# Optimization experiments

Hardware: AMD Instinct MI355X
Metric: run time of the kernel (lower is better)

## Reference

```python
import jax, jax.numpy as jnp
import numpy as np

# Model dims (scaled Mistral-style decoder)
L = 2        # layers
D = 2048     # d_model
H = 16       # query heads
HK = 4       # kv heads (GQA)
HD = 128     # head dim
F = 8192     # SwiGLU hidden
V = 32000    # vocab
R = 64       # LoRA rank
BATCH = 16
S = 128
BLK = 64             # NF4 quant blocksize
SCALE = 128.0 / 64.0  # lora_alpha / r
THETA = 10000.0
EPS = 1e-5

# bitsandbytes NF4 codebook (16 levels)
NF4 = jnp.array([-1.0, -0.6961928009986877, -0.5250730514526367, -0.39491748809814453,
                 -0.28444138169288635, -0.18477343022823334, -0.09105003625154495, 0.0,
                 0.07958029955625534, 0.16093020141124725, 0.24611230194568634,
                 0.33791524171829224, 0.44070982933044434, 0.5626170039176941,
                 0.7229568362236023, 1.0], dtype=jnp.float32)


def _dequant(codes, absmax):
    # codes: [out, in] int codes 0..15; absmax: [out, in//BLK] per-block scale
    o, i = codes.shape
    w = NF4[codes].reshape(o, i // BLK, BLK) * absmax[:, :, None]
    return w.reshape(o, i)


def _qlinear(x, codes, absmax, A, Bm):
    # fused NF4 dequant + GEMM + LoRA delta: y = x W^T + scale * (x A^T) B^T
    return x @ _dequant(codes, absmax).T + SCALE * ((x @ A.T) @ Bm.T)


def _rms(x, w):
    return x * jax.lax.rsqrt(jnp.mean(x * x, axis=-1, keepdims=True) + EPS) * w


def _rope(x):
    # x: [B, S, heads, HD]; rotate-half RoPE
    half = HD // 2
    inv = 1.0 / (THETA ** (jnp.arange(half, dtype=jnp.float32) / half))
    ang = jnp.arange(x.shape[1], dtype=jnp.float32)[:, None] * inv[None, :]  # [S, half]
    cos = jnp.cos(ang)[None, :, None, :]
    sin = jnp.sin(ang)[None, :, None, :]
    x1, x2 = x[..., :half], x[..., half:]
    return jnp.concatenate([x1 * cos - x2 * sin, x2 * cos + x1 * sin], axis=-1)


def reference(input_ids, attention_mask, embed, attn_norm_w, mlp_norm_w, final_norm_w,
              q_codes, q_absmax, q_A, q_B, k_codes, k_absmax, k_A, k_B,
              v_codes, v_absmax, v_A, v_B, o_codes, o_absmax, o_A, o_B,
              gate_codes, gate_absmax, gate_A, gate_B, up_codes, up_absmax, up_A, up_B,
              down_codes, down_absmax, down_A, down_B):
    b, s = input_ids.shape
    h = embed[input_ids]  # [B, S, D]
    causal = jnp.tril(jnp.ones((s, s), dtype=bool))
    keep = causal[None, None, :, :] & (attention_mask[:, None, None, :] > 0)
    bias = jnp.where(keep, 0.0, -1e9).astype(h.dtype)
    for l in range(L):
        x = _rms(h, attn_norm_w[l])
        q = _qlinear(x, q_codes[l], q_absmax[l], q_A[l], q_B[l]).reshape(b, s, H, HD)
        k = _qlinear(x, k_codes[l], k_absmax[l], k_A[l], k_B[l]).reshape(b, s, HK, HD)
        v = _qlinear(x, v_codes[l], v_absmax[l], v_A[l], v_B[l]).reshape(b, s, HK, HD)
        q = _rope(q)
        k = _rope(k)
        k = jnp.repeat(k, H // HK, axis=2)  # GQA expand
        v = jnp.repeat(v, H // HK, axis=2)
        scores = jnp.einsum('bqhd,bkhd->bhqk', q, k) / jnp.sqrt(jnp.float32(HD)) + bias
        attn = jax.nn.softmax(scores, axis=-1)
        ctx = jnp.einsum('bhqk,bkhd->bqhd', attn, v).reshape(b, s, D)
        h = h + _qlinear(ctx, o_codes[l], o_absmax[l], o_A[l], o_B[l])
        x = _rms(h, mlp_norm_w[l])
        g = _qlinear(x, gate_codes[l], gate_absmax[l], gate_A[l], gate_B[l])
        u = _qlinear(x, up_codes[l], up_absmax[l], up_A[l], up_B[l])
        h = h + _qlinear(jax.nn.silu(g) * u, down_codes[l], down_absmax[l], down_A[l], down_B[l])
    h = _rms(h, final_norm_w)
    # last-token pooling: gather hidden state at sum(mask)-1 (normalized=False)
    seq_len = jnp.sum(attention_mask, axis=1) - 1
    return h[jnp.arange(b), seq_len]


def setup_inputs() -> dict:
    key = jax.random.key(0)
    ks = iter(jax.random.split(key, 64))
    def codes(shape):
        return jax.random.randint(next(ks), shape, 0, 16, dtype=jnp.int32)
    def absm(o, i):
        return jax.random.uniform(next(ks), (L, o, i // BLK), dtype=jnp.float32) * 0.05
    def lora(o, i):
        A = jax.random.normal(next(ks), (L, R, i), dtype=jnp.float32) * 0.02
        Bm = jax.random.normal(next(ks), (L, o, R), dtype=jnp.float32) * 0.02
        return A, Bm
    inp = {
        'input_ids': jax.random.randint(next(ks), (BATCH, S), 0, V, dtype=jnp.int32),
        'attention_mask': jnp.ones((BATCH, S), dtype=jnp.int32),
        'embed': jax.random.normal(next(ks), (V, D), dtype=jnp.float32) * 0.02,
        'attn_norm_w': jnp.ones((L, D), jnp.float32),
        'mlp_norm_w': jnp.ones((L, D), jnp.float32),
        'final_norm_w': jnp.ones((D,), jnp.float32),
    }
    dims = {'q': (D, D), 'k': (HK * HD, D), 'v': (HK * HD, D), 'o': (D, D),
            'gate': (F, D), 'up': (F, D), 'down': (D, F)}
    for name, (o, i) in dims.items():
        A, Bm = lora(o, i)
        inp[f'{name}_codes'] = codes((L, o, i))
        inp[f'{name}_absmax'] = absm(o, i)
        inp[f'{name}_A'] = A
        inp[f'{name}_B'] = Bm
    return inp
```

## Files before the change

### kernel.cpp

```cpp
#include <hip/hip_runtime.h>
#include <stdint.h>

#define D_ 2048
#define H_ 16
#define HK_ 4
#define F_ 8192
#define R_ 64
#define NTOK_ 2048
#define EPS_ 1e-5f

typedef unsigned short u16;
typedef short short8 __attribute__((ext_vector_type(8)));
typedef float f32x4 __attribute__((ext_vector_type(4)));

__constant__ float NF4_TAB[16] = {
  -1.0f, -0.6961928009986877f, -0.5250730514526367f, -0.39491748809814453f,
  -0.28444138169288635f, -0.18477343022823334f, -0.09105003625154495f, 0.0f,
  0.07958029955625534f, 0.16093020141124725f, 0.24611230194568634f, 0.33791524171829224f,
  0.44070982933044434f, 0.5626170039176941f, 0.7229568362236023f, 1.0f };

static __device__ __forceinline__ float b2f(u16 u){ return __uint_as_float(((unsigned)u)<<16); }
static __device__ __forceinline__ u16 f2b(float f){
  unsigned u = __float_as_uint(f);
  return (u16)((u + 0x7fffu + ((u>>16)&1u)) >> 16);
}

__global__ void k_embed(const int* __restrict__ ids, const float* __restrict__ embed,
                        float* __restrict__ h){
  int tok = blockIdx.x;
  int id  = ids[tok];
  const float4* src = (const float4*)(embed + (size_t)id * D_);
  float4* dst = (float4*)(h + (size_t)tok * D_);
  for (int i = threadIdx.x; i < D_/4; i += 256) dst[i] = src[i];
}

__global__ void k_rms(const float* __restrict__ h, const float* __restrict__ w,
                      u16* __restrict__ xb){
  __shared__ float red[4];
  int row = blockIdx.x, t = threadIdx.x;
  const float* hr = h + (size_t)row * D_;
  float ss = 0.f;
  for (int i = t; i < D_; i += 256){ float v = hr[i]; ss += v*v; }
  #pragma unroll
  for (int m = 32; m; m >>= 1) ss += __shfl_xor(ss, m, 64);
  if ((t & 63) == 0) red[t >> 6] = ss;
  __syncthreads();
  float sc = rsqrtf((red[0]+red[1]+red[2]+red[3]) * (1.0f/D_) + EPS_);
  for (int i = t; i < D_; i += 256) xb[(size_t)row*D_ + i] = f2b(hr[i]*sc*w[i]);
}

struct FoldSet { const int* c; const float* am; const float* A; const float* Bm; u16* W; };

static __device__ __forceinline__ void fold_tile(const int* __restrict__ codes,
    const float* __restrict__ absmax, const float* __restrict__ Amat,
    const float* __restrict__ Bmat, u16* __restrict__ W, int I, int n0, int k0){
  __shared__ float Cl[64*132];
  __shared__ float nf4s[16];
  u16* At = (u16*)Cl;
  u16* Bl = (u16*)Cl + 128*64;
  int t = threadIdx.x;
  if (t < 16) nf4s[t] = NF4_TAB[t];
  #pragma unroll
  for (int it = 0; it < 8; ++it){
    int fi = it*256 + t;
    int r = fi >> 5, c4 = fi & 31;
    float4 v = *(const float4*)(Amat + (size_t)r*I + k0 + c4*4);
    int kc0 = c4*4;
    At[((kc0+0)*64 + r) ^ (((kc0+0)&7)<<3)] = f2b(v.x);
    At[((kc0+1)*64 + r) ^ (((kc0+1)&7)<<3)] = f2b(v.y);
    At[((kc0+2)*64 + r) ^ (((kc0+2)&7)<<3)] = f2b(v.z);
    At[((kc0+3)*64 + r) ^ (((kc0+3)&7)<<3)] = f2b(v.w);
  }
  #pragma unroll
  for (int it = 0; it < 8; ++it){
    int fi = it*256 + t;
    int nl = fi >> 4, r4 = fi & 15;
    float4 v = *(const float4*)(Bmat + (size_t)(n0+nl)*R_ + r4*4);
    uint2 p; p.x = (unsigned)f2b(v.x) | ((unsigned)f2b(v.y)<<16);
    p.y = (unsigned)f2b(v.z) | ((unsigned)f2b(v.w)<<16);
    *(uint2*)&Bl[(nl*64 + r4*4) ^ ((nl&7)<<3)] = p;
  }
  __syncthreads();
  int w = t >> 6, lane = t & 63;
  int lr = lane & 15, lg = lane >> 4;
  f32x4 acc[2][8];
  #pragma unroll
  for (int mt = 0; mt < 2; ++mt)
    #pragma unroll
    for (int nt = 0; nt < 8; ++nt) acc[mt][nt] = (f32x4){0.f,0.f,0.f,0.f};
  #pragma unroll
  for (int ks = 0; ks < 64; ks += 32){
    short8 af[2], bf_[8];
    #pragma unroll
    for (int mt = 0; mt < 2; ++mt)
      af[mt] = *(const short8*)&At[((w*32 + mt*16 + lr)*64 + ks + lg*8) ^ ((lr&7)<<3)];
    #pragma unroll
    for (int nt = 0; nt < 8; ++nt)
      bf_[nt] = *(const short8*)&Bl[((nt*16 + lr)*64 + ks + lg*8) ^ ((lr&7)<<3)];
    #pragma unroll
    for (int mt = 0; mt < 2; ++mt)
      #pragma unroll
      for (int nt = 0; nt < 8; ++nt)
        acc[mt][nt] = __builtin_amdgcn_mfma_f32_16x16x32_bf16(af[mt], bf_[nt], acc[mt][nt], 0, 0, 0);
  }
  int tk = t & 15, tn2 = t >> 4;
  int Ib = I >> 6;
  int kcb = k0 + tk*8;
  int kblk = kcb >> 6;
  #pragma unroll
  for (int half = 0; half < 2; ++half){
    __syncthreads();
    #pragma unroll
    for (int mt = 0; mt < 2; ++mt)
      #pragma unroll
      for (int nt2 = 0; nt2 < 4; ++nt2)
        *(f32x4*)&Cl[(nt2*16 + lr)*132 + w*32 + mt*16 + lg*4] = acc[mt][half*4 + nt2];
    __syncthreads();
    #pragma unroll
    for (int j = 0; j < 4; ++j){
      int nl = tn2*4 + j;
      int n = n0 + half*64 + nl;
      float am = absmax[(size_t)n*Ib + kblk];
      int4 c0 = *(const int4*)(codes + (size_t)n*I + kcb);
      int4 c1 = *(const int4*)(codes + (size_t)n*I + kcb + 4);
      const float* L = &Cl[nl*132 + tk*8];
      u16 o[8];
      o[0]=f2b(nf4s[c0.x&15]*am + 2.0f*L[0]);
      o[1]=f2b(nf4s[c0.y&15]*am + 2.0f*L[1]);
      o[2]=f2b(nf4s[c0.z&15]*am + 2.0f*L[2]);
      o[3]=f2b(nf4s[c0.w&15]*am + 2.0f*L[3]);
      o[4]=f2b(nf4s[c1.x&15]*am + 2.0f*L[4]);
      o[5]=f2b(nf4s[c1.y&15]*am + 2.0f*L[5]);
      o[6]=f2b(nf4s[c1.z&15]*am + 2.0f*L[6]);
      o[7]=f2b(nf4s[c1.w&15]*am + 2.0f*L[7]);
      uint4 pk;
      pk.x=(unsigned)o[0]|((unsigned)o[1]<<16); pk.y=(unsigned)o[2]|((unsigned)o[3]<<16);
      pk.z=(unsigned)o[4]|((unsigned)o[5]<<16); pk.w=(unsigned)o[6]|((unsigned)o[7]<<16);
      *(uint4*)(W + (size_t)n*I + kcb) = pk;
    }
  }
}

__global__ __launch_bounds__(256) void k_fold3(FoldSet a, FoldSet b, FoldSet c,
                                               int y1, int y2, int I){
  int y = blockIdx.y;
  FoldSet s = (y < y1) ? a : (y < y2) ? b : c;
  int n0 = (y < y1) ? y*128 : (y < y2) ? (y-y1)*128 : (y-y2)*128;
  fold_tile(s.c, s.am, s.A, s.Bm, s.W, I, n0, blockIdx.x*128);
}

#define LDW_ 40
template<int EPI>
__global__ __launch_bounds__(256,3) void k_gemm(const u16* __restrict__ A,
      const u16* __restrict__ B, float* __restrict__ Cf, u16* __restrict__ C0,
      u16* __restrict__ C1, u16* __restrict__ C2, int M, int N, int K){
  __shared__ u16 SA[2][128*LDW_];
  __shared__ u16 SB[2][128*LDW_];
  int t = threadIdx.x;
  int n0 = blockIdx.x*128, m0 = blockIdx.y*128;
  int w = t >> 6, lane = t & 63;
  int mw = (w >> 1)*64, nw = (w & 1)*64;
  int lr = lane & 15, lg = lane >> 4;
  f32x4 acc[4][4];
  #pragma unroll
  for (int mt = 0; mt < 4; ++mt)
    #pragma unroll
    for (int nt = 0; nt < 4; ++nt) acc[mt][nt] = (f32x4){0.f,0.f,0.f,0.f};
  const u16* Ag = A + (size_t)(m0 + (t>>2))*K + (t&3)*8;
  const u16* Bg = B + (size_t)(n0 + (t>>2))*K + (t&3)*8;
  int trow = t >> 2, tcol = (t & 3)*8;
  int wof0 = trow*LDW_ + tcol;
  int wof1 = (64 + trow)*LDW_ + tcol;
  int niter = K >> 5;

  uint4 ra0, ra1, rb0, rb1;
  uint4 sa0, sa1, sb0, sb1;
  auto gload = [&](int it, uint4& a0, uint4& a1, uint4& b0, uint4& b1){
    int kb = it*32;
    a0 = *(const uint4*)(Ag + kb);
    a1 = *(const uint4*)(Ag + (size_t)64*K + kb);
    b0 = *(const uint4*)(Bg + kb);
    b1 = *(const uint4*)(Bg + (size_t)64*K + kb);
  };
  gload(0, ra0, ra1, rb0, rb1);
  gload(1, sa0, sa1, sb0, sb1);

  auto step = [&](int buf, uint4& a0, uint4& a1, uint4& b0, uint4& b1, int pf){
    *(uint4*)&SA[buf][wof0] = a0;
    *(uint4*)&SA[buf][wof1] = a1;
    *(uint4*)&SB[buf][wof0] = b0;
    *(uint4*)&SB[buf][wof1] = b1;
    __builtin_amdgcn_s_waitcnt(0xC07F);
    __builtin_amdgcn_s_barrier();
    gload(pf, a0, a1, b0, b1);
    short8 af[4], bf_[4];
    #pragma unroll
    for (int mt = 0; mt < 4; ++mt) af[mt]  = *(const short8*)&SA[buf][(mw + mt*16 + lr)*LDW_ + lg*8];
    #pragma unroll
    for (int nt = 0; nt < 4; ++nt) bf_[nt] = *(const short8*)&SB[buf][(nw + nt*16 + lr)*LDW_ + lg*8];
    #pragma unroll
    for (int mt = 0; mt < 4; ++mt)
      #pragma unroll
      for (int nt = 0; nt < 4; ++nt)
        acc[mt][nt] = __builtin_amdgcn_mfma_f32_16x16x32_bf16(af[mt], bf_[nt], acc[mt][nt], 0, 0, 0);
  };

  for (int k = 0; k < niter; k += 2){
    step(0, ra0, ra1, rb0, rb1, (k+2 < niter) ? k+2 : k);
    step(1, sa0, sa1, sb0, sb1, (k+3 < niter) ? k+3 : k+1);
  }

  u16* cb_ = C0; int ldc = N; int coff = n0;
  if (EPI == 2){
    if (n0 < 2048)      { cb_ = C0; ldc = 2048; coff = n0; }
    else if (n0 < 2560) { cb_ = C1; ldc = 512;  coff = n0 - 2048; }
    else                { cb_ = C2; ldc = 512;  coff = n0 - 2560; }
  }
  if (EPI == 3){
    if (n0 < 512)       { cb_ = C1; ldc = 512;  coff = n0; }
    else                { cb_ = C2; ldc = 512;  coff = n0 - 512; }
  }
  #pragma unroll
  for (int mt = 0; mt < 4; ++mt)
    #pragma unroll
    for (int nt = 0; nt < 4; ++nt){
      int cl = nw + nt*16 + lr;
      #pragma unroll
      for (int rg = 0; rg < 4; ++rg){
        int row = m0 + mw + mt*16 + lg*4 + rg;
        float v = acc[mt][nt][rg];
        if (EPI == 1){
          Cf[(size_t)row*N + n0 + cl] += v;
        } else if (EPI == 4){
          size_t idx = (size_t)row*ldc + coff + cl;
          float g = b2f(C1[idx]);
          cb_[idx] = f2b((g/(1.0f+__expf(-g)))*v);
        } else {
          cb_[(size_t)row*ldc + coff + cl] = f2b(v);
        }
      }
    }
}

template<int OUT, int GA, int KC>
__global__ __launch_bounds__(256) void k_skinny(const u16* __restrict__ A,
      const u16* __restrict__ B, float* __restrict__ Hf, u16* __restrict__ Cb,
      const int* __restrict__ rows, int N, int K){
  int w = threadIdx.x >> 6, lane = threadIdx.x & 63;
  int lr = lane & 15, lg = lane >> 4;
  int n0 = blockIdx.x*64 + w*16;
  int kbase = blockIdx.y * KC;
  int ar = GA ? rows[lr] : lr;
  f32x4 ac0 = (f32x4){0.f,0.f,0.f,0.f};
  f32x4 ac1 = (f32x4){0.f,0.f,0.f,0.f};
  const u16* Ap = A + (size_t)ar*K + kbase + lg*8;
  const u16* Bp = B + (size_t)(n0 + lr)*K + kbase + lg*8;
  #pragma unroll 8
  for (int k = 0; k < KC; k += 64){
    ac0 = __builtin_amdgcn_mfma_f32_16x16x32_bf16(*(const short8*)(Ap + k),
            *(const short8*)(Bp + k), ac0, 0, 0, 0);
    ac1 = __builtin_amdgcn_mfma_f32_16x16x32_bf16(*(const short8*)(Ap + k + 32),
            *(const short8*)(Bp + k + 32), ac1, 0, 0, 0);
  }
  f32x4 acc = ac0 + ac1;
  #pragma unroll
  for (int rg = 0; rg < 4; ++rg){
    int m = lg*4 + rg;
    if (OUT == 0){
      Cb[(size_t)m*N + n0 + lr] = f2b(acc[rg]);
    } else if (OUT == 1){
      atomicAdd(&Hf[(size_t)rows[m]*D_ + n0 + lr], acc[rg]);
    } else {
      size_t idx = (size_t)m*N + n0 + lr;
      float g = b2f(Cb[idx]);
      Cb[idx] = f2b((g/(1.0f+__expf(-g)))*acc[rg]);
    }
  }
}

__global__ void k_rows(const int* __restrict__ mask, int* __restrict__ rows){
  int b = threadIdx.x;
  if (b < 16){
    int c = 0;
    for (int i = 0; i < 128; ++i) c += (mask[b*128+i] > 0);
    rows[b] = b*128 + c - 1;
  }
}

__global__ void k_rms16(const float* __restrict__ h, const float* __restrict__ w,
                        const int* __restrict__ rows, u16* __restrict__ xq){
  __shared__ float red[4];
  int m = blockIdx.x, t = threadIdx.x;
  const float* hr = h + (size_t)rows[m] * D_;
  float ss = 0.f;
  for (int i = t; i < D_; i += 256){ float v = hr[i]; ss += v*v; }
  #pragma unroll
  for (int mm = 32; mm; mm >>= 1) ss += __shfl_xor(ss, mm, 64);
  if ((t & 63) == 0) red[t >> 6] = ss;
  __syncthreads();
  float sc = rsqrtf((red[0]+red[1]+red[2]+red[3]) * (1.0f/D_) + EPS_);
  for (int i = t; i < D_; i += 256) xq[(size_t)m*D_ + i] = f2b(hr[i]*sc*w[i]);
}

__global__ void k_rope(u16* __restrict__ x, int nh){
  int i = blockIdx.x*256 + threadIdx.x;
  int d = i & 63; int rem = i >> 6; int hh = rem % nh; int tok = rem / nh;
  int s = tok & 127;
  size_t base = (size_t)tok*nh*128 + hh*128 + d;
  float x1 = b2f(x[base]), x2 = b2f(x[base+64]);
  float inv = exp2f(-(float)d * 0.20762050581352868f);
  float ang = (float)s * inv;
  float sn = sinf(ang), cs = cosf(ang);
  x[base]      = f2b(x1*cs - x2*sn);
  x[base+64]   = f2b(x2*cs + x1*sn);
}

__global__ void k_rope16(u16* __restrict__ x, const int* __restrict__ rows){
  int i = blockIdx.x*256 + threadIdx.x;
  int d = i & 63; int hh = (i >> 6) & 15; int m = i >> 10;
  int s = rows[m] & 127;
  size_t base = (size_t)m*2048 + hh*128 + d;
  float x1 = b2f(x[base]), x2 = b2f(x[base+64]);
  float inv = exp2f(-(float)d * 0.20762050581352868f);
  float ang = (float)s * inv;
  float sn = sinf(ang), cs = cosf(ang);
  x[base]      = f2b(x1*cs - x2*sn);
  x[base+64]   = f2b(x2*cs + x1*sn);
}

#define ALD_ 132
__global__ __launch_bounds__(256) void k_attn(const u16* __restrict__ q,
      const u16* __restrict__ kk, const u16* __restrict__ vv,
      const int* __restrict__ mask, u16* __restrict__ ctx){
  __shared__ u16 QP[128*ALD_];
  __shared__ u16 KV[128*ALD_];
  int b = blockIdx.y, h = blockIdx.x;
  int t = threadIdx.x, w = t >> 6, lane = t & 63;
  int lr = lane & 15, lg = lane >> 4;
  #pragma unroll
  for (int it = 0; it < 8; ++it){
    int fi = it*256 + t; int s = fi >> 4, c8 = fi & 15;
    *(uint4*)&QP[s*ALD_ + c8*8] = *(const uint4*)(q  + (size_t)(b*128+s)*2048 + h*128 + c8*8);
    *(uint4*)&KV[s*ALD_ + c8*8] = *(const uint4*)(kk + (size_t)(b*128+s)*512 + (h>>2)*128 + c8*8);
  }
  __syncthreads();
  f32x4 sac[2][8];
  #pragma unroll
  for (int mt = 0; mt < 2; ++mt)
    #pragma unroll
    for (int nt = 0; nt < 8; ++nt) sac[mt][nt] = (f32x4){0.f,0.f,0.f,0.f};
  for (int ks = 0; ks < 128; ks += 32){
    short8 a[2], bb[8];
    #pragma unroll
    for (int mt = 0; mt < 2; ++mt) a[mt] = *(const short8*)&QP[(w*32 + mt*16 + lr)*ALD_ + ks + lg*8];
    #pragma unroll
    for (int nt = 0; nt < 8; ++nt) bb[nt] = *(const short8*)&KV[(nt*16 + lr)*ALD_ + ks + lg*8];
    #pragma unroll
    for (int mt = 0; mt < 2; ++mt)
      #pragma unroll
      for (int nt = 0; nt < 8; ++nt)
        sac[mt][nt] = __builtin_amdgcn_mfma_f32_16x16x32_bf16(a[mt], bb[nt], sac[mt][nt], 0, 0, 0);
  }
  const float NEG = -1e9f, scl = 0.08838834764831845f;
  float mbias[8];
  #pragma unroll
  for (int nt = 0; nt < 8; ++nt) mbias[nt] = (mask[b*128 + nt*16 + lr] > 0) ? 0.f : NEG;
  #pragma unroll
  for (int mt = 0; mt < 2; ++mt)
    #pragma unroll
    for (int rg = 0; rg < 4; ++rg){
      int row = w*32 + mt*16 + lg*4 + rg;
      float vvv[8]; float mx = -3e38f;
      #pragma unroll
      for (int nt = 0; nt < 8; ++nt){
        int col = nt*16 + lr;
        float s_ = sac[mt][nt][rg]*scl + ((col <= row) ? mbias[nt] : NEG);
        vvv[nt] = s_; mx = fmaxf(mx, s_);
      }
      #pragma unroll
      for (int m_ = 1; m_ < 16; m_ <<= 1) mx = fmaxf(mx, __shfl_xor(mx, m_, 64));
      float sum = 0.f;
      #pragma unroll
      for (int nt = 0; nt < 8; ++nt){ vvv[nt] = __expf(vvv[nt]-mx); sum += vvv[nt]; }
      #pragma unroll
      for (int m_ = 1; m_ < 16; m_ <<= 1) sum += __shfl_xor(sum, m_, 64);
      float inv = 1.0f/sum;
      #pragma unroll
      for (int nt = 0; nt < 8; ++nt) QP[row*ALD_ + nt*16 + lr] = f2b(vvv[nt]*inv);
    }
  __syncthreads();
  #pragma unroll
  for (int it = 0; it < 8; ++it){
    int fi = it*256 + t; int s = fi >> 4, c8 = fi & 15;
    u16 tmp[8];
    *(uint4*)tmp = *(const uint4*)(vv + (size_t)(b*128+s)*512 + (h>>2)*128 + c8*8);
    #pragma unroll
    for (int j = 0; j < 8; ++j) KV[(c8*8+j)*ALD_ + s] = tmp[j];
  }
  __syncthreads();
  f32x4 oac[2][8];
  #pragma unroll
  for (int mt = 0; mt < 2; ++mt)
    #pragma unroll
    for (int nt = 0; nt < 8; ++nt) oac[mt][nt] = (f32x4){0.f,0.f,0.f,0.f};
  for (int ks = 0; ks < 128; ks += 32){
    short8 a[2], bb[8];
    #pragma unroll
    for (int mt = 0; mt < 2; ++mt) a[mt] = *(const short8*)&QP[(w*32 + mt*16 + lr)*ALD_ + ks + lg*8];
    #pragma unroll
    for (int nt = 0; nt < 8; ++nt) bb[nt] = *(const short8*)&KV[(nt*16 + lr)*ALD_ + ks + lg*8];
    #pragma unroll
    for (int mt = 0; mt < 2; ++mt)
      #pragma unroll
      for (int nt = 0; nt < 8; ++nt)
        oac[mt][nt] = __builtin_amdgcn_mfma_f32_16x16x32_bf16(a[mt], bb[nt], oac[mt][nt], 0, 0, 0);
  }
  #pragma unroll
  for (int mt = 0; mt < 2; ++mt)
    #pragma unroll
    for (int nt = 0; nt < 8; ++nt)
      #pragma unroll
      for (int rg = 0; rg < 4; ++rg){
        int row = w*32 + mt*16 + lg*4 + rg;
        int col = nt*16 + lr;
        ctx[(size_t)(b*128+row)*2048 + h*128 + col] = f2b(oac[mt][nt][rg]);
      }
}

__global__ void k_attn1(const u16* __restrict__ qc, const u16* __restrict__ kk,
      const u16* __restrict__ vv, const int* __restrict__ mask,
      const int* __restrict__ rows, u16* __restrict__ out){
  __shared__ float ps[128];
  __shared__ float red2[2];
  int h = blockIdx.x, b = blockIdx.y, t = threadIdx.x;
  int pos = rows[b] & 127;
  const u16* qrow = qc + (size_t)b*2048 + h*128;
  const u16* krow = kk + (size_t)(b*128 + t)*512 + (h>>2)*128;
  float acc = 0.f;
  #pragma unroll
  for (int d0 = 0; d0 < 128; d0 += 8){
    short8 qa = *(const short8*)(qrow + d0);
    short8 ka = *(const short8*)(krow + d0);
    #pragma unroll
    for (int j = 0; j < 8; ++j) acc += b2f((u16)qa[j]) * b2f((u16)ka[j]);
  }
  bool keep = (t <= pos) && (mask[b*128 + t] > 0);
  float s_ = keep ? acc * 0.08838834764831845f : -1e9f;
  float mx = s_;
  #pragma unroll
  for (int m_ = 1; m_ < 64; m_ <<= 1) mx = fmaxf(mx, __shfl_xor(mx, m_, 64));
  if ((t & 63) == 0) red2[t >> 6] = mx;
  __syncthreads();
  mx = fmaxf(red2[0], red2[1]);
  float p = __expf(s_ - mx);
  float sum = p;
  #pragma unroll
  for (int m_ = 1; m_ < 64; m_ <<= 1) sum += __shfl_xor(sum, m_, 64);
  __syncthreads();
  if ((t & 63) == 0) red2[t >> 6] = sum;
  __syncthreads();
  float inv = 1.f / (red2[0] + red2[1]);
  ps[t] = p * inv;
  __syncthreads();
  float o = 0.f;
  const u16* vbase = vv + (size_t)b*128*512 + (h>>2)*128 + t;
  for (int s = 0; s < 128; s += 4){
    o += ps[s]   * b2f(vbase[(size_t)(s  )*512]);
    o += ps[s+1] * b2f(vbase[(size_t)(s+1)*512]);
    o += ps[s+2] * b2f(vbase[(size_t)(s+2)*512]);
    o += ps[s+3] * b2f(vbase[(size_t)(s+3)*512]);
  }
  out[(size_t)b*2048 + h*128 + t] = f2b(o);
}

__global__ void k_final(const float* __restrict__ h, const int* __restrict__ mask,
                        const float* __restrict__ w, float* __restrict__ out){
  __shared__ float red[4]; __shared__ int rowsh;
  int b = blockIdx.x, t = threadIdx.x;
  if (t == 0){
    int c = 0;
    for (int i = 0; i < 128; ++i) c += (mask[b*128+i] > 0);
    rowsh = b*128 + c - 1;
  }
  __syncthreads();
  const float* hr = h + (size_t)rowsh*D_;
  float ss = 0.f;
  for (int i = t; i < D_; i += 256){ float x = hr[i]; ss += x*x; }
  #pragma unroll
  for (int m = 32; m; m >>= 1) ss += __shfl_xor(ss, m, 64);
  if ((t & 63) == 0) red[t >> 6] = ss;
  __syncthreads();
  float sc = rsqrtf((red[0]+red[1]+red[2]+red[3]) * (1.0f/D_) + EPS_);
  for (int i = t; i < D_; i += 256) out[(size_t)b*D_ + i] = hr[i]*sc*w[i];
}

extern "C" void kernel_launch(void* const* d_in, const int* in_sizes, int n_in,
                              void* d_out, int out_size, void* d_ws, size_t ws_size,
                              hipStream_t stream) {
  const int*   ids       = (const int*)  d_in[0];
  const int*   mask      = (const int*)  d_in[1];
  const float* embed     = (const float*)d_in[2];
  const float* attn_norm = (const float*)d_in[3];
  const float* mlp_norm  = (const float*)d_in[4];
  const float* fin_norm  = (const float*)d_in[5];
  struct QW { const int* c; const float* am; const float* A; const float* B; };
  auto qw = [&](int i){ return QW{(const int*)d_in[i], (const float*)d_in[i+1],
                                  (const float*)d_in[i+2], (const float*)d_in[i+3]}; };
  QW Wq = qw(6), Wk = qw(10), Wv = qw(14), Wo = qw(18), Wg = qw(22), Wu = qw(26), Wd = qw(30);

  char* ws = (char*)d_ws;
  float* h  = (float*)(ws);
  u16* xb   = (u16*)(ws + 16777216);
  u16* qb   = (u16*)(ws + 25165824);
  u16* kb_  = (u16*)(ws + 33554432);
  u16* vb   = (u16*)(ws + 35651584);
  u16* gb   = (u16*)(ws + 37748736);
  u16* Wb   = (u16*)(ws + 104857600);
  int* rowsi = (int*)(ws + 138412032);
  u16* xq    = (u16*)(ws + 138413056);
  u16* qc    = (u16*)(ws + 138478592);
  u16* cc    = (u16*)(ws + 138544128);
  u16* g16   = (u16*)(ws + 138609664);
  u16* Wb2   = (u16*)(ws + 167772160);

  auto fs = [&](QW W_, int l, int O, int I, u16* dst){
    return FoldSet{ W_.c + (size_t)l*O*I, W_.am + (size_t)l*O*(I>>6),
                    W_.A + (size_t)l*R_*I, W_.B + (size_t)l*O*R_, dst };
  };

  k_embed<<<NTOK_, 256, 0, stream>>>(ids, embed, h);

  for (int l = 0; l < 2; ++l){
    k_rms<<<NTOK_, 256, 0, stream>>>(h, attn_norm + l*D_, xb);
    {
      FoldSet fq = fs(Wq, l, D_, D_, Wb);
      FoldSet fk = fs(Wk, l, 512, D_, Wb + (size_t)2048*D_);
      FoldSet fv = fs(Wv, l, 512, D_, Wb + (size_t)2560*D_);
      k_fold3<<<dim3(16,24), 256, 0, stream>>>(fq, fk, fv, 16, 20, D_);
    }

    if (l == 0){
      k_gemm<2><<<dim3(24,16), 256, 0, stream>>>(xb, Wb, nullptr, qb, kb_, vb, NTOK_, 3072, D_);
      k_rope<<<8192, 256, 0, stream>>>(qb, H_);
      k_rope<<<2048, 256, 0, stream>>>(kb_, HK_);
      k_attn<<<dim3(16,16), 256, 0, stream>>>(qb, kb_, vb, mask, xb);
      {
        FoldSet fo = fs(Wo, l, D_, D_, Wb);
        k_fold3<<<dim3(16,16), 256, 0, stream>>>(fo, fo, fo, 9999, 9999, D_);
      }
      k_gemm<1><<<dim3(16,16), 256, 0, stream>>>(xb, Wb, h, nullptr, nullptr, nullptr, NTOK_, D_, D_);
      k_rms<<<NTOK_, 256, 0, stream>>>(h, mlp_norm + l*D_, xb);
      {
        FoldSet fg = fs(Wg, l, F_, D_, Wb);
        FoldSet fu = fs(Wu, l, F_, D_, Wb2);
        k_fold3<<<dim3(16,128), 256, 0, stream>>>(fg, fu, fu, 64, 64, D_);
      }
      k_gemm<0><<<dim3(64,16), 256, 0, stream>>>(xb, Wb,  nullptr, gb, nullptr, nullptr, NTOK_, F_, D_);
      k_gemm<4><<<dim3(64,16), 256, 0, stream>>>(xb, Wb2, nullptr, gb, gb, nullptr, NTOK_, F_, D_);
      {
        FoldSet fd = fs(Wd, l, D_, F_, Wb);
        k_fold3<<<dim3(64,16), 256, 0, stream>>>(fd, fd, fd, 9999, 9999, F_);
      }
      k_gemm<1><<<dim3(16,16), 256, 0, stream>>>(gb, Wb, h, nullptr, nullptr, nullptr, NTOK_, D_, F_);
    } else {
      k_gemm<3><<<dim3(8,16), 256, 0, stream>>>(xb, Wb + (size_t)2048*D_, nullptr, nullptr,
          kb_, vb, NTOK_, 1024, D_);
      k_rows<<<1, 64, 0, stream>>>(mask, rowsi);
      k_skinny<0,1,2048><<<dim3(32,1), 256, 0, stream>>>(xb, Wb, nullptr, qc, rowsi, D_, D_);
      k_rope16<<<64, 256, 0, stream>>>(qc, rowsi);
      k_rope<<<2048, 256, 0, stream>>>(kb_, HK_);
      k_attn1<<<dim3(16,16), 128, 0, stream>>>(qc, kb_, vb, mask, rowsi, cc);
      {
        FoldSet fo = fs(Wo, l, D_, D_, Wb);
        k_fold3<<<dim3(16,16), 256, 0, stream>>>(fo, fo, fo, 9999, 9999, D_);
      }
      k_skinny<1,0,2048><<<dim3(32,1), 256, 0, stream>>>(cc, Wb, h, nullptr, rowsi, D_, D_);
      k_rms16<<<16, 256, 0, stream>>>(h, mlp_norm + l*D_, rowsi, xq);
      {
        FoldSet fg = fs(Wg, l, F_, D_, Wb);
        FoldSet fu = fs(Wu, l, F_, D_, Wb2);
        k_fold3<<<dim3(16,128), 256, 0, stream>>>(fg, fu, fu, 64, 64, D_);
      }
      k_skinny<0,0,2048><<<dim3(128,1), 256, 0, stream>>>(xq, Wb,  nullptr, g16, rowsi, F_, D_);
      k_skinny<3,0,2048><<<dim3(128,1), 256, 0, stream>>>(xq, Wb2, nullptr, g16, rowsi, F_, D_);
      {
        FoldSet fd = fs(Wd, l, D_, F_, Wb);
        k_fold3<<<dim3(64,16), 256, 0, stream>>>(fd, fd, fd, 9999, 9999, F_);
      }
      k_skinny<1,0,2048><<<dim3(32,4), 256, 0, stream>>>(g16, Wb, h, nullptr, rowsi, D_, F_);
    }
  }
  k_final<<<16, 256, 0, stream>>>(h, mask, fin_norm, (float*)d_out);
}
```

Before: 1.303 ms.

## Add 256x256-tile double-buffered GEMM for layer-0 gate/up projections

Adds a new bf16 MFMA GEMM kernel that uses 256x256 output tiles with 512 threads and a double-buffered, XOR-swizzled LDS layout. Global loads for the next k-step are prefetched into registers while the current step computes, and MFMA issue is wrapped in s_setprio. The layer-0 gate and up GEMMs, including the SiLU-multiply epilogue, now use this kernel, and the EPI==4 path is removed from the old GEMM. The aim is more reuse per LDS load and better latency hiding on the largest GEMMs, at the cost of one block per CU under high register and LDS pressure.

```diff
diff --git a/kernel.cpp b/kernel.cpp
--- a/kernel.cpp
+++ b/kernel.cpp
@@ -231,12 +231,112 @@
         float v = acc[mt][nt][rg];
         if (EPI == 1){
           Cf[(size_t)row*N + n0 + cl] += v;
-        } else if (EPI == 4){
-          size_t idx = (size_t)row*ldc + coff + cl;
-          float g = b2f(C1[idx]);
-          cb_[idx] = f2b((g/(1.0f+__expf(-g)))*v);
         } else {
           cb_[(size_t)row*ldc + coff + cl] = f2b(v);
+        }
+      }
+    }
+}
+
+template<int EPI>
+__global__ __launch_bounds__(512,1) void k_gemm256(const u16* __restrict__ A,
+      const u16* __restrict__ B, u16* __restrict__ C0, const u16* __restrict__ C1,
+      int M, int N, int K){
+  __shared__ u16 LB[2][2][256*64];
+  int t = threadIdx.x;
+  int w = t >> 6, l = t & 63;
+  int wm = w >> 2, wn = w & 3;
+  int lr = l & 15, lg = l >> 4;
+  int ls = l >> 3;
+  int lc = (l & 7)*8;
+  int n0 = blockIdx.x*256, m0 = blockIdx.y*256;
+  f32x4 acc[8][4];
+  #pragma unroll
+  for (int i = 0; i < 8; ++i)
+    #pragma unroll
+    for (int j = 0; j < 4; ++j) acc[i][j] = (f32x4){0.f,0.f,0.f,0.f};
+
+  const u16* Ag = A + (size_t)(m0 + w*8 + ls)*K + lc;
+  const u16* Bg = B + (size_t)(n0 + w*8 + ls)*K + lc;
+  int wrow = w*8 + ls;
+  int wcol = lc ^ ((ls & 7) << 3);
+  int nk = K >> 6;
+
+  uint4 rA[4], rB[4];
+  auto gload = [&](int kt){
+    #pragma unroll
+    for (int i = 0; i < 4; ++i){
+      rA[i] = *(const uint4*)(Ag + (size_t)i*64*K + kt*64);
+      rB[i] = *(const uint4*)(Bg + (size_t)i*64*K + kt*64);
+    }
+  };
+  gload(0);
+
+  for (int kt = 0; kt < nk; ++kt){
+    int buf = kt & 1;
+    u16* As = &LB[buf][0][0];
+    u16* Bs = &LB[buf][1][0];
+    #pragma unroll
+    for (int i = 0; i < 4; ++i){
+      *(uint4*)&As[(i*64 + wrow)*64 + wcol] = rA[i];
+      *(uint4*)&Bs[(i*64 + wrow)*64 + wcol] = rB[i];
+    }
+    __builtin_amdgcn_s_waitcnt(0xC07F);
+    __builtin_amdgcn_s_barrier();
+    gload(kt+1 < nk ? kt+1 : kt);
+
+    short8 aF[4][2], bF[2][2];
+    auto loadA = [&](int pm){
+      #pragma unroll
+      for (int mf = 0; mf < 4; ++mf){
+        int row = wm*128 + pm*64 + mf*16 + lr;
+        #pragma unroll
+        for (int ks = 0; ks < 2; ++ks)
+          aF[mf][ks] = *(const short8*)&As[row*64 + ((ks*32 + lg*8) ^ ((row&7)<<3))];
+      }
+    };
+    auto loadB = [&](int pn){
+      #pragma unroll
+      for (int nf = 0; nf < 2; ++nf){
+        int row = wn*64 + pn*32 + nf*16 + lr;
+        #pragma unroll
+        for (int ks = 0; ks < 2; ++ks)
+          bF[nf][ks] = *(const short8*)&Bs[row*64 + ((ks*32 + lg*8) ^ ((row&7)<<3))];
+      }
+    };
+    auto mma = [&](int pm, int pn){
+      __builtin_amdgcn_s_setprio(1);
+      #pragma unroll
+      for (int mf = 0; mf < 4; ++mf)
+        #pragma unroll
+        for (int nf = 0; nf < 2; ++nf)
+          #pragma unroll
+          for (int ks = 0; ks < 2; ++ks)
+            acc[pm*4+mf][pn*2+nf] = __builtin_amdgcn_mfma_f32_16x16x32_bf16(
+                aF[mf][ks], bF[nf][ks], acc[pm*4+mf][pn*2+nf], 0, 0, 0);
+      __builtin_amdgcn_s_setprio(0);
+    };
+    loadA(0); loadB(0); mma(0, 0);
+    loadA(1);           mma(1, 0);
+    loadB(1);           mma(1, 1);
+    loadA(0);           mma(0, 1);
+  }
+
+  #pragma unroll
+  for (int mf8 = 0; mf8 < 8; ++mf8)
+    #pragma unroll
+    for (int nf4 = 0; nf4 < 4; ++nf4){
+      int col = n0 + wn*64 + nf4*16 + lr;
+      #pragma unroll
+      for (int rg = 0; rg < 4; ++rg){
+        int row = m0 + wm*128 + mf8*16 + lg*4 + rg;
+        size_t idx = (size_t)row*N + col;
+        float v = acc[mf8][nf4][rg];
+        if (EPI == 4){
+          float g = b2f(C1[idx]);
+          C0[idx] = f2b((g/(1.0f+__expf(-g)))*v);
+        } else {
+          C0[idx] = f2b(v);
         }
       }
     }
@@ -555,8 +655,8 @@
         FoldSet fu = fs(Wu, l, F_, D_, Wb2);
         k_fold3<<<dim3(16,128), 256, 0, stream>>>(fg, fu, fu, 64, 64, D_);
       }
-      k_gemm<0><<<dim3(64,16), 256, 0, stream>>>(xb, Wb,  nullptr, gb, nullptr, nullptr, NTOK_, F_, D_);
-      k_gemm<4><<<dim3(64,16), 256, 0, stream>>>(xb, Wb2, nullptr, gb, gb, nullptr, NTOK_, F_, D_);
+      k_gemm256<0><<<dim3(32,8), 512, 0, stream>>>(xb, Wb,  gb, nullptr, NTOK_, F_, D_);
+      k_gemm256<4><<<dim3(32,8), 512, 0, stream>>>(xb, Wb2, gb, gb,      NTOK_, F_, D_);
       {
         FoldSet fd = fs(Wd, l, D_, F_, Wb);
         k_fold3<<<dim3(64,16), 256, 0, stream>>>(fd, fd, fd, 9999, 9999, F_);
```

New measurement: 1.363 ms. 4.5% more time.
